# Kernel tuning notes

Hardware: AMD Instinct MI355X
Metric: run time of the kernel (lower is better)

Reference implementation:

```python
import jax, jax.numpy as jnp
import numpy as np

B, S, H = 2, 4096, 2048
NH, NKV, D = 16, 4, 128
BS, LOCAL, GLOB, STRIDE = 64, 8, 4, 16
SEL = GLOB + LOCAL
SCALE = D ** -0.5
NEG = -1e9


def rotate_half(x):
    x1, x2 = x[..., : D // 2], x[..., D // 2 :]
    return jnp.concatenate([-x2, x1], axis=-1)


def setup_inputs():
    key = jax.random.key(0)
    ks = jax.random.split(key, 5)
    hidden_states = jax.random.normal(ks[0], (B, S, H), dtype=jnp.float32)
    # standard RoPE tables, shape [B, S, D] as the module expects (cos.unsqueeze(1))
    pos = jnp.arange(S, dtype=jnp.float32)
    inv = 1.0 / (10000.0 ** (jnp.arange(0, D, 2, dtype=jnp.float32) / D))
    freqs = pos[:, None] * inv[None, :]
    emb = jnp.concatenate([freqs, freqs], axis=-1)
    cos = jnp.broadcast_to(jnp.cos(emb)[None], (B, S, D)).astype(jnp.float32)
    sin = jnp.broadcast_to(jnp.sin(emb)[None], (B, S, D)).astype(jnp.float32)
    std = 0.02
    Wq = jax.random.normal(ks[1], (NH * D, H), dtype=jnp.float32) * std
    Wk = jax.random.normal(ks[2], (NKV * D, H), dtype=jnp.float32) * std
    Wv = jax.random.normal(ks[3], (NKV * D, H), dtype=jnp.float32) * std
    Wo = jax.random.normal(ks[4], (H, NH * D), dtype=jnp.float32) * std
    return {"hidden_states": hidden_states, "cos": cos, "sin": sin,
            "Wq": Wq, "Wk": Wk, "Wv": Wv, "Wo": Wo}


def _block_sparse_attn(q, k, v):
    # q, k, v: [B, NH, S, D]; past_len = 0, attention_mask = None (all keys valid)
    qb = S // BS
    kb = S // BS
    qid = jnp.arange(qb)
    # local blocks: the LOCAL most recent blocks ending at the query block
    loc = qid[:, None] - (LOCAL - 1 - jnp.arange(LOCAL)[None, :])
    loc = jnp.clip(loc, 0, kb - 1)
    # global blocks: strided anchors
    g = jnp.clip(jnp.arange(GLOB) * STRIDE, 0, kb - 1)
    glob = jnp.broadcast_to(g[None, :], (qb, GLOB))
    sel = jnp.concatenate([glob, loc], axis=1)  # [qb, SEL]
    valid = sel <= qid[:, None]                 # causal at block level
    # dedup: drop a selected block if an earlier slot selected the same block
    eq = sel[:, :, None] == sel[:, None, :]
    lower = jnp.tril(jnp.ones((SEL, SEL), dtype=bool), k=-1)
    keep = (~(eq & lower[None]).any(-1)) & valid  # [qb, SEL]

    k_blk = k.reshape(B, NH, kb, BS, D)
    v_blk = v.reshape(B, NH, kb, BS, D)
    k_sel = jnp.take(k_blk, sel.reshape(-1), axis=2).reshape(B, NH, qb, SEL * BS, D)
    v_sel = jnp.take(v_blk, sel.reshape(-1), axis=2).reshape(B, NH, qb, SEL * BS, D)
    q_blk = q.reshape(B, NH, qb, BS, D)

    scores = jnp.einsum("bhqid,bhqjd->bhqij", q_blk, k_sel) * SCALE  # [B,NH,qb,BS,SEL*BS]
    keep_tok = jnp.broadcast_to(keep[:, :, None], (qb, SEL, BS)).reshape(qb, SEL * BS)
    scores = scores + (1.0 - keep_tok.astype(scores.dtype))[None, None, :, None, :] * NEG
    # intra-block causal mask where selected block == query block
    same = (sel == qid[:, None]).astype(scores.dtype)  # [qb, SEL]
    intra = jnp.triu(jnp.full((BS, BS), NEG, dtype=scores.dtype), k=1)
    scores6 = scores.reshape(B, NH, qb, BS, SEL, BS)
    scores6 = scores6 + intra[None, None, None, :, None, :] * same[None, None, :, None, :, None]
    scores = scores6.reshape(B, NH, qb, BS, SEL * BS)
    probs = jax.nn.softmax(scores, axis=-1)
    out = jnp.einsum("bhqij,bhqjd->bhqid", probs, v_sel)
    return out.reshape(B, NH, S, D)


def reference(hidden_states, cos, sin, Wq, Wk, Wv, Wo):
    q = (hidden_states @ Wq.T).reshape(B, S, NH, D).transpose(0, 2, 1, 3)
    k = (hidden_states @ Wk.T).reshape(B, S, NKV, D).transpose(0, 2, 1, 3)
    v = (hidden_states @ Wv.T).reshape(B, S, NKV, D).transpose(0, 2, 1, 3)
    c = cos[:, None, :, :]
    s = sin[:, None, :, :]
    q = q * c + rotate_half(q) * s
    k = k * c + rotate_half(k) * s
    rep = NH // NKV
    k = jnp.repeat(k, rep, axis=1)
    v = jnp.repeat(v, rep, axis=1)
    out = _block_sparse_attn(q, k, v)
    out = out.transpose(0, 2, 1, 3).reshape(B, S, NH * D)
    return out @ Wo.T
```

## Files before the change

kernel.cpp:

```cpp
#include <hip/hip_runtime.h>

typedef __bf16 bf16_t;
typedef __bf16 bf16x8_t __attribute__((ext_vector_type(8)));
typedef __bf16 bf16x4_t __attribute__((ext_vector_type(4)));
typedef float f32x4_t __attribute__((ext_vector_type(4)));
typedef unsigned short u16;
typedef unsigned int u32;

#define B_ 2
#define S_ 4096
#define NH_ 16
#define NKV_ 4
#define D_ 128
#define NEG_ (-1000000000.0f)
#define SCALE_ 0.08838834764831845f

__device__ __forceinline__ void load16(const bf16_t* g, bf16_t* l) {
  __builtin_amdgcn_global_load_lds(
      (__attribute__((address_space(1))) void*)(g),
      (__attribute__((address_space(3))) void*)(l),
      16, 0, 0);
}

__global__ __launch_bounds__(256) void cvt_all_kernel(const float* __restrict__ hs,
                                                      const float* __restrict__ Wq,
                                                      const float* __restrict__ Wk,
                                                      const float* __restrict__ Wv,
                                                      const float* __restrict__ Wo,
                                                      bf16_t* __restrict__ Xb,
                                                      bf16_t* __restrict__ Wb,
                                                      bf16_t* __restrict__ Wob) {
  int i = blockIdx.x * 256 + threadIdx.x;
  const float* src; bf16_t* dst; int local;
  if (i < 4194304)      { src = hs; dst = Xb;            local = i; }
  else if (i < 5242880) { src = Wq; dst = Wb;            local = i - 4194304; }
  else if (i < 5505024) { src = Wk; dst = Wb + 4194304;  local = i - 5242880; }
  else if (i < 5767168) { src = Wv; dst = Wb + 5242880;  local = i - 5505024; }
  else                  { src = Wo; dst = Wob;           local = i - 5767168; }
  float4 v = ((const float4*)src)[local];
  bf16x4_t o;
  o.x = (bf16_t)v.x; o.y = (bf16_t)v.y; o.z = (bf16_t)v.z; o.w = (bf16_t)v.w;
  *(bf16x4_t*)(dst + (size_t)local * 4) = o;
}

template <int BF16OUT>
__global__ __launch_bounds__(256) void gemm_bt_kernel(const bf16_t* __restrict__ A,
                                                      const bf16_t* __restrict__ Bm,
                                                      float* __restrict__ Cf,
                                                      bf16_t* __restrict__ Cb,
                                                      int M, int N, int K) {
  __shared__ bf16_t As[128 * 32];
  __shared__ bf16_t Bs[128 * 32];
  const int t = threadIdx.x;
  const int lane = t & 63;
  const int w = t >> 6;
  const int wr = w >> 1, wc = w & 1;
  const int l15 = lane & 15, l4 = lane >> 4;
  const int m0 = blockIdx.x * 128;
  const int n0 = blockIdx.y * 128;
  const int xr = (l15 >> 1) & 3;

  f32x4_t acc[4][4] = {};

  for (int k0 = 0; k0 < K; k0 += 32) {
    __syncthreads();
#pragma unroll
    for (int i = 0; i < 2; i++) {
      int f = t + 256 * i;
      int row = f >> 2, cl = f & 3;
      int cg = cl ^ ((row >> 1) & 3);
      load16(A + (size_t)(m0 + row) * K + k0 + cg * 8, As + (w * 64 + i * 256) * 8);
      load16(Bm + (size_t)(n0 + row) * K + k0 + cg * 8, Bs + (w * 64 + i * 256) * 8);
    }
    __syncthreads();
    bf16x8_t af[4], bfr[4];
#pragma unroll
    for (int mi = 0; mi < 4; mi++) {
      int ra = wr * 64 + mi * 16 + l15;
      af[mi] = *(const bf16x8_t*)&As[(ra * 4 + (l4 ^ xr)) * 8];
    }
#pragma unroll
    for (int ni = 0; ni < 4; ni++) {
      int rb = wc * 64 + ni * 16 + l15;
      bfr[ni] = *(const bf16x8_t*)&Bs[(rb * 4 + (l4 ^ xr)) * 8];
    }
#pragma unroll
    for (int mi = 0; mi < 4; mi++)
#pragma unroll
      for (int ni = 0; ni < 4; ni++)
        acc[mi][ni] = __builtin_amdgcn_mfma_f32_16x16x32_bf16(af[mi], bfr[ni], acc[mi][ni], 0, 0, 0);
  }

#pragma unroll
  for (int mi = 0; mi < 4; mi++)
#pragma unroll
    for (int ni = 0; ni < 4; ni++)
#pragma unroll
      for (int r = 0; r < 4; r++) {
        int grow = m0 + wr * 64 + mi * 16 + l4 * 4 + r;
        int gcol = n0 + wc * 64 + ni * 16 + l15;
        float v = acc[mi][ni][r];
        if (BF16OUT) Cb[(size_t)grow * N + gcol] = (bf16_t)v;
        else Cf[(size_t)grow * N + gcol] = v;
      }
}

__global__ __launch_bounds__(320) void rope_kernel(const bf16_t* __restrict__ qkv,
                                                   const float* __restrict__ cosp,
                                                   const float* __restrict__ sinp,
                                                   bf16_t* __restrict__ Qro,
                                                   bf16_t* __restrict__ Kro) {
  const int tk = blockIdx.x;
  const int b = tk >> 12;
  const int s = tk & 4095;
  const int sblock = s >> 6, row = s & 63;
  const int idx = threadIdx.x;
  int head, lc;
  const bf16_t* base;
  bf16_t* outp;
  if (idx < 256) {
    head = idx >> 4; lc = idx & 15;
    base = qkv + (size_t)tk * 3072 + head * 128;
    outp = Qro + ((size_t)(b * NH_ + head) * 64 + sblock) * 8192;
  } else {
    int i2 = idx - 256;
    head = i2 >> 4; lc = i2 & 15;
    base = qkv + (size_t)tk * 3072 + 2048 + head * 128;
    outp = Kro + ((size_t)(b * NKV_ + head) * 64 + sblock) * 8192;
  }
  const int d0 = lc * 8;
  bf16x8_t x = *(const bf16x8_t*)(base + d0);
  const int d0p = (d0 < 64) ? d0 + 64 : d0 - 64;
  bf16x8_t xp = *(const bf16x8_t*)(base + d0p);
  const float sgn = (d0 < 64) ? -1.0f : 1.0f;
  const float* cb = cosp + (size_t)tk * 128 + d0;
  const float* sb = sinp + (size_t)tk * 128 + d0;
  bf16x8_t o;
#pragma unroll
  for (int e = 0; e < 8; e++)
    o[e] = (bf16_t)((float)x[e] * cb[e] + sgn * (float)xp[e] * sb[e]);
  *(bf16x8_t*)(outp + (lc * 64 + row) * 8) = o;
}

__global__ __launch_bounds__(256) void vtrans_kernel(const u16* __restrict__ qkv,
                                                     u16* __restrict__ vt) {
  __shared__ u16 tile[64][136];
  const int sblock = blockIdx.x;
  const int kh = blockIdx.y;
  const int b = blockIdx.z;
  const int t = threadIdx.x;
#pragma unroll
  for (int i = 0; i < 4; i++) {
    int f = t + 256 * i;
    int sl = f >> 4, c = f & 15;
    uint4 vv = *(const uint4*)(qkv + (size_t)(b * S_ + sblock * 64 + sl) * 3072 + 2560 + kh * 128 + c * 8);
    *(uint4*)&tile[sl][c * 8] = vv;
  }
  __syncthreads();
  u16* out = vt + ((size_t)(b * NKV_ + kh) * 64 + sblock) * 8192;
#pragma unroll
  for (int i = 0; i < 4; i++) {
    int g = t + 256 * i;
    int sc = g >> 7, d = g & 127;
    u16 e0 = tile[sc * 8 + 0][d], e1 = tile[sc * 8 + 1][d];
    u16 e2 = tile[sc * 8 + 2][d], e3 = tile[sc * 8 + 3][d];
    u16 e4 = tile[sc * 8 + 4][d], e5 = tile[sc * 8 + 5][d];
    u16 e6 = tile[sc * 8 + 6][d], e7 = tile[sc * 8 + 7][d];
    uint4 ov;
    ov.x = (u32)e0 | ((u32)e1 << 16);
    ov.y = (u32)e2 | ((u32)e3 << 16);
    ov.z = (u32)e4 | ((u32)e5 << 16);
    ov.w = (u32)e6 | ((u32)e7 << 16);
    *(uint4*)(out + (size_t)g * 8) = ov;
  }
}

__global__ __launch_bounds__(256) void attn_kernel(const bf16_t* __restrict__ Qr,
                                                   const bf16_t* __restrict__ Kr,
                                                   const bf16_t* __restrict__ Vt,
                                                   bf16_t* __restrict__ Ao) {
  __shared__ bf16_t Ks[2][8192];
  __shared__ bf16_t Vs[2][8192];
  __shared__ bf16_t Ps[4 * 16 * 72];
  const int qid = blockIdx.x;
  const int kh = blockIdx.y >> 1;
  const int hp = blockIdx.y & 1;
  const int b = blockIdx.z;
  const int t = threadIdx.x;
  const int lane = t & 63;
  const int w = t >> 6;
  const int l15 = lane & 15, l4 = lane >> 4;
  const int h = kh * 4 + hp * 2 + (w >> 1);
  int row0[2];
  row0[0] = ((w * 2) & 3) * 16;
  row0[1] = ((w * 2 + 1) & 3) * 16;

  int list[12];
  int nkeep = 0;
#pragma unroll
  for (int j = 0; j < 12; j++) {
    int cj;
    if (j < 4) cj = j * 16;
    else { cj = qid - 11 + j; cj = cj < 0 ? 0 : cj; cj = cj > 63 ? 63 : cj; }
    bool keep = (cj <= qid);
#pragma unroll
    for (int i = 0; i < j; i++) {
      int ci;
      if (i < 4) ci = i * 16;
      else { ci = qid - 11 + i; ci = ci < 0 ? 0 : ci; ci = ci > 63 ? 63 : ci; }
      if (ci == cj) keep = false;
    }
    if (keep) list[nkeep++] = cj;
  }

  const bf16_t* Qg = Qr + ((size_t)(b * NH_ + h) * 64 + qid) * 8192;
  const bf16_t* Kg = Kr + ((size_t)(b * NKV_ + kh) * 64) * 8192;
  const bf16_t* Vg = Vt + ((size_t)(b * NKV_ + kh) * 64) * 8192;

  bf16x8_t qa[2][4];
#pragma unroll
  for (int mt = 0; mt < 2; mt++)
#pragma unroll
    for (int ks = 0; ks < 4; ks++)
      qa[mt][ks] = *(const bf16x8_t*)(Qg + ((ks * 4 + l4) * 64 + row0[mt] + l15) * 8);

  bf16x8_t ones;
#pragma unroll
  for (int e = 0; e < 8; e++) ones[e] = (bf16_t)1.0f;

  float mi_r[2][4], li_r[2][4];
  f32x4_t oacc[2][8] = {};
#pragma unroll
  for (int mt = 0; mt < 2; mt++)
#pragma unroll
    for (int r = 0; r < 4; r++) { mi_r[mt][r] = -__builtin_inff(); li_r[mt][r] = 0.0f; }

  {
    int cj = list[0];
#pragma unroll
    for (int i = 0; i < 4; i++) {
      int f = t + 256 * i;
      load16(Kg + (size_t)cj * 8192 + (size_t)f * 8, Ks[0] + (w * 64 + i * 256) * 8);
      load16(Vg + (size_t)cj * 8192 + (size_t)f * 8, Vs[0] + (w * 64 + i * 256) * 8);
    }
  }

  int cur = 0;
#pragma unroll 1
  for (int idx = 0; idx < nkeep; idx++) {
    const int cj = list[idx];
    __syncthreads();
    if (idx + 1 < nkeep) {
      int cn = list[idx + 1];
#pragma unroll
      for (int i = 0; i < 4; i++) {
        int f = t + 256 * i;
        load16(Kg + (size_t)cn * 8192 + (size_t)f * 8, Ks[cur ^ 1] + (w * 64 + i * 256) * 8);
        load16(Vg + (size_t)cn * 8192 + (size_t)f * 8, Vs[cur ^ 1] + (w * 64 + i * 256) * 8);
      }
    }
    const bf16_t* ks_ = Ks[cur];
    const bf16_t* vs_ = Vs[cur];

    f32x4_t sacc[2][4] = {};
#pragma unroll
    for (int ks = 0; ks < 4; ks++)
#pragma unroll
      for (int ni = 0; ni < 4; ni++) {
        bf16x8_t kb = *(const bf16x8_t*)&ks_[((ks * 4 + l4) * 64 + ni * 16 + l15) * 8];
#pragma unroll
        for (int mt = 0; mt < 2; mt++)
          sacc[mt][ni] = __builtin_amdgcn_mfma_f32_16x16x32_bf16(qa[mt][ks], kb, sacc[mt][ni], 0, 0, 0);
      }

    const bool diag = (cj == qid);
    float alpha[2][4];
#pragma unroll
    for (int mt = 0; mt < 2; mt++) {
      float sv[4][4];
#pragma unroll
      for (int ni = 0; ni < 4; ni++)
#pragma unroll
        for (int r = 0; r < 4; r++) {
          float x = sacc[mt][ni][r] * SCALE_;
          if (diag && (ni * 16 + l15) > (row0[mt] + l4 * 4 + r)) x += NEG_;
          sv[ni][r] = x;
        }

      float rmax[4];
#pragma unroll
      for (int r = 0; r < 4; r++)
        rmax[r] = fmaxf(fmaxf(sv[0][r], sv[1][r]), fmaxf(sv[2][r], sv[3][r]));
#pragma unroll
      for (int msk = 1; msk < 16; msk <<= 1)
#pragma unroll
        for (int r = 0; r < 4; r++)
          rmax[r] = fmaxf(rmax[r], __shfl_xor(rmax[r], msk, 64));
#pragma unroll
      for (int r = 0; r < 4; r++) {
        float nm = fmaxf(mi_r[mt][r], rmax[r]);
        alpha[mt][r] = __expf(mi_r[mt][r] - nm);
        mi_r[mt][r] = nm;
      }
      float p[4][4];
#pragma unroll
      for (int ni = 0; ni < 4; ni++)
#pragma unroll
        for (int r = 0; r < 4; r++)
          p[ni][r] = __expf(sv[ni][r] - mi_r[mt][r]);
#pragma unroll
      for (int ni = 0; ni < 4; ni++)
#pragma unroll
        for (int r = 0; r < 4; r++)
          Ps[w * 1152 + (l4 * 4 + r) * 72 + ni * 16 + l15] = (bf16_t)p[ni][r];
#pragma unroll
      for (int n2 = 0; n2 < 8; n2++)
#pragma unroll
        for (int r = 0; r < 4; r++)
          oacc[mt][n2][r] *= alpha[mt][r];

      f32x4_t lacc = {};
#pragma unroll
      for (int kst = 0; kst < 2; kst++) {
        bf16x8_t pa = *(const bf16x8_t*)&Ps[w * 1152 + l15 * 72 + kst * 32 + l4 * 8];
        lacc = __builtin_amdgcn_mfma_f32_16x16x32_bf16(pa, ones, lacc, 0, 0, 0);
#pragma unroll
        for (int n2 = 0; n2 < 8; n2++) {
          bf16x8_t vb = *(const bf16x8_t*)&vs_[((kst * 4 + l4) * 128 + n2 * 16 + l15) * 8];
          oacc[mt][n2] = __builtin_amdgcn_mfma_f32_16x16x32_bf16(pa, vb, oacc[mt][n2], 0, 0, 0);
        }
      }
#pragma unroll
      for (int r = 0; r < 4; r++)
        li_r[mt][r] = li_r[mt][r] * alpha[mt][r] + lacc[r];
    }

    cur ^= 1;
  }

#pragma unroll
  for (int mt = 0; mt < 2; mt++) {
    float invl[4];
#pragma unroll
    for (int r = 0; r < 4; r++) invl[r] = 1.0f / li_r[mt][r];
#pragma unroll
    for (int n2 = 0; n2 < 8; n2++)
#pragma unroll
      for (int r = 0; r < 4; r++) {
        int m = row0[mt] + l4 * 4 + r;
        size_t idx = ((size_t)(b * S_ + qid * 64 + m)) * (NH_ * D_) + h * D_ + n2 * 16 + l15;
        Ao[idx] = (bf16_t)(oacc[mt][n2][r] * invl[r]);
      }
  }
}

extern "C" void kernel_launch(void* const* d_in, const int* in_sizes, int n_in,
                              void* d_out, int out_size, void* d_ws, size_t ws_size,
                              hipStream_t stream) {
  const float* hs = (const float*)d_in[0];
  const float* cosp = (const float*)d_in[1];
  const float* sinp = (const float*)d_in[2];
  const float* Wq = (const float*)d_in[3];
  const float* Wk = (const float*)d_in[4];
  const float* Wv = (const float*)d_in[5];
  const float* Wo = (const float*)d_in[6];
  float* outp = (float*)d_out;

  char* ws = (char*)d_ws;
  bf16_t* Xb   = (bf16_t*)(ws);
  bf16_t* Wb   = (bf16_t*)(ws + 33554432);
  bf16_t* Wob  = (bf16_t*)(ws + 46137344);
  bf16_t* QKVo = (bf16_t*)(ws + 54525952);
  bf16_t* Qr   = (bf16_t*)(ws + 104857600);
  bf16_t* Kr   = (bf16_t*)(ws + 138412032);
  bf16_t* Vt   = (bf16_t*)(ws + 146800640);
  bf16_t* Ao   = QKVo;

  cvt_all_kernel<<<dim3(26624), dim3(256), 0, stream>>>(hs, Wq, Wk, Wv, Wo, Xb, Wb, Wob);

  gemm_bt_kernel<1><<<dim3(64, 24), dim3(256), 0, stream>>>(Xb, Wb, (float*)nullptr, QKVo,
                                                            8192, 3072, 2048);
  rope_kernel<<<dim3(8192), dim3(320), 0, stream>>>(QKVo, cosp, sinp, Qr, Kr);
  vtrans_kernel<<<dim3(64, NKV_, B_), dim3(256), 0, stream>>>((const u16*)QKVo, (u16*)Vt);
  attn_kernel<<<dim3(64, NKV_ * 2, B_), dim3(256), 0, stream>>>(Qr, Kr, Vt, Ao);
  gemm_bt_kernel<0><<<dim3(64, 16), dim3(256), 0, stream>>>(Ao, Wob, outp, (bf16_t*)nullptr,
                                                            8192, 2048, 2048);
}
```

Before: 531.8 us.

## Replace 128x128 GEMM with 256x256 double-buffered pipelined 8-wave kernel

Replaces the simple single-buffered 128x128 GEMM used for the QKV projection and the output projection with a 256x256-tile, 512-thread kernel. It double-buffers LDS over 64-wide K steps and interleaves global-to-LDS staging with MFMA quadrants under explicit barriers and setprio. It also remaps workgroups across XCDs so neighbouring tiles share an L2. The goal is more data reuse per tile and hiding load latency behind matrix math. In exchange it uses more registers and LDS, drops the old LDS swizzle, and relies on hand-tuned waitcnt counts that are fragile.

```diff
diff --git a/kernel.cpp b/kernel.cpp
--- a/kernel.cpp
+++ b/kernel.cpp
@@ -43,63 +43,124 @@
   *(bf16x4_t*)(dst + (size_t)local * 4) = o;
 }
 
+
+#define SB0() __builtin_amdgcn_sched_barrier(0)
+#define BAR_MID() { SB0(); __builtin_amdgcn_s_barrier(); \
+  asm volatile("s_waitcnt lgkmcnt(0)" ::: "memory"); SB0(); }
+#define BAR_END() { SB0(); __builtin_amdgcn_s_barrier(); SB0(); }
+#define BAR_END_VM() { SB0(); asm volatile("s_waitcnt vmcnt(4)" ::: "memory"); \
+  __builtin_amdgcn_s_barrier(); SB0(); }
+
+#define LDA_(BUF, MP) { \
+  _Pragma("unroll") for (int mi = 0; mi < 4; mi++) { \
+    _Pragma("unroll") for (int ks = 0; ks < 2; ks++) { \
+      a[mi][ks] = *(const bf16x8_t*)&As[BUF][ks][wr * 128 + (MP) * 64 + mi * 16 + l15][l4 * 8]; } } }
+
+#define LDB_(BUF, NP) { \
+  _Pragma("unroll") for (int n2 = 0; n2 < 2; n2++) { \
+    _Pragma("unroll") for (int ks = 0; ks < 2; ks++) { \
+      b[(NP) * 2 + n2][ks] = *(const bf16x8_t*)&Bs[BUF][ks][wc * 64 + (NP) * 32 + n2 * 16 + l15][l4 * 8]; } } }
+
+#define MFMA_Q(MP, NP) { \
+  __builtin_amdgcn_s_setprio(1); \
+  _Pragma("unroll") for (int mi = 0; mi < 4; mi++) { \
+    _Pragma("unroll") for (int n2 = 0; n2 < 2; n2++) { \
+      _Pragma("unroll") for (int ks = 0; ks < 2; ks++) { \
+        acc[(MP) * 4 + mi][(NP) * 2 + n2] = __builtin_amdgcn_mfma_f32_16x16x32_bf16( \
+            a[mi][ks], b[(NP) * 2 + n2][ks], acc[(MP) * 4 + mi][(NP) * 2 + n2], 0, 0, 0); } } } \
+  __builtin_amdgcn_s_setprio(0); }
+
 template <int BF16OUT>
-__global__ __launch_bounds__(256) void gemm_bt_kernel(const bf16_t* __restrict__ A,
-                                                      const bf16_t* __restrict__ Bm,
-                                                      float* __restrict__ Cf,
-                                                      bf16_t* __restrict__ Cb,
-                                                      int M, int N, int K) {
-  __shared__ bf16_t As[128 * 32];
-  __shared__ bf16_t Bs[128 * 32];
+__global__ __launch_bounds__(512, 2) void gemm256_kernel(const bf16_t* __restrict__ A,
+                                                         const bf16_t* __restrict__ Bm,
+                                                         float* __restrict__ Cf,
+                                                         bf16_t* __restrict__ Cb,
+                                                         int M, int N, int K) {
+  __shared__ __align__(16) bf16_t As[2][2][256][32];
+  __shared__ __align__(16) bf16_t Bs[2][2][256][32];
   const int t = threadIdx.x;
   const int lane = t & 63;
   const int w = t >> 6;
-  const int wr = w >> 1, wc = w & 1;
+  const int wr = w >> 2;
+  const int wc = w & 3;
   const int l15 = lane & 15, l4 = lane >> 4;
-  const int m0 = blockIdx.x * 128;
-  const int n0 = blockIdx.y * 128;
-  const int xr = (l15 >> 1) & 3;
-
-  f32x4_t acc[4][4] = {};
-
-  for (int k0 = 0; k0 < K; k0 += 32) {
-    __syncthreads();
-#pragma unroll
-    for (int i = 0; i < 2; i++) {
-      int f = t + 256 * i;
-      int row = f >> 2, cl = f & 3;
-      int cg = cl ^ ((row >> 1) & 3);
-      load16(A + (size_t)(m0 + row) * K + k0 + cg * 8, As + (w * 64 + i * 256) * 8);
-      load16(Bm + (size_t)(n0 + row) * K + k0 + cg * 8, Bs + (w * 64 + i * 256) * 8);
-    }
-    __syncthreads();
-    bf16x8_t af[4], bfr[4];
-#pragma unroll
-    for (int mi = 0; mi < 4; mi++) {
-      int ra = wr * 64 + mi * 16 + l15;
-      af[mi] = *(const bf16x8_t*)&As[(ra * 4 + (l4 ^ xr)) * 8];
-    }
-#pragma unroll
-    for (int ni = 0; ni < 4; ni++) {
-      int rb = wc * 64 + ni * 16 + l15;
-      bfr[ni] = *(const bf16x8_t*)&Bs[(rb * 4 + (l4 ^ xr)) * 8];
-    }
-#pragma unroll
-    for (int mi = 0; mi < 4; mi++)
-#pragma unroll
-      for (int ni = 0; ni < 4; ni++)
-        acc[mi][ni] = __builtin_amdgcn_mfma_f32_16x16x32_bf16(af[mi], bfr[ni], acc[mi][ni], 0, 0, 0);
-  }
-
-#pragma unroll
-  for (int mi = 0; mi < 4; mi++)
+  const int sp = w >> 2;
+  const int swi = w & 3;
+  const int srow = lane >> 2;
+  const int sg = lane & 3;
+
+  const int nwg = gridDim.x;
+  const int qq = nwg >> 3, rr = nwg & 7;
+  const int xcd = blockIdx.x & 7, bix = blockIdx.x >> 3;
+  const int wg = (xcd < rr ? xcd * (qq + 1) : rr * (qq + 1) + (xcd - rr) * qq) + bix;
+  const int mtiles = M >> 8;
+  const int m0 = (wg % mtiles) * 256;
+  const int n0 = (wg / mtiles) * 256;
+
+  const bf16_t* Ablk = A + (size_t)m0 * K;
+  const bf16_t* Bblk = Bm + (size_t)n0 * K;
+
+  f32x4_t acc[8][4] = {};
+  bf16x8_t a[4][2], b[4][2];
+
+  const int nkt = K >> 6;
+  const int nit = nkt >> 1;
+
+  auto stageA = [&](int buf, int mp, int kt) {
+#pragma unroll
+    for (int c = 0; c < 2; c++) {
+      int r0 = c * 128 + mp * 64;
+      load16(Ablk + (size_t)(r0 + swi * 16 + srow) * K + kt * 64 + sp * 32 + sg * 8,
+             &As[buf][0][0][0] + sp * 8192 + (r0 + swi * 16) * 32);
+    }
+  };
+  auto stageB = [&](int buf, int np, int kt) {
+#pragma unroll
+    for (int c = 0; c < 2; c++) {
+      int r0 = (c * 2 + (swi >> 1)) * 64 + np * 32 + (swi & 1) * 16;
+      load16(Bblk + (size_t)(r0 + srow) * K + kt * 64 + sp * 32 + sg * 8,
+             &Bs[buf][0][0][0] + sp * 8192 + r0 * 32);
+    }
+  };
+
+  stageA(0, 0, 0); stageB(0, 0, 0); stageA(0, 1, 0); stageB(0, 1, 0);
+  stageA(1, 0, 1); stageB(1, 0, 1);
+  asm volatile("s_waitcnt vmcnt(4)" ::: "memory");
+  __builtin_amdgcn_s_barrier();
+  SB0();
+
+#pragma unroll 1
+  for (int i = 0; i < nit; i++) {
+    const int ktA = 2 * i + 1;
+    const int ktB = (2 * i + 2 < nkt) ? 2 * i + 2 : nkt - 1;
+    const int ktC = (2 * i + 3 < nkt) ? 2 * i + 3 : nkt - 1;
+    LDA_(0, 0); LDB_(0, 0); stageA(1, 1, ktA);
+    BAR_MID(); MFMA_Q(0, 0); BAR_END();
+    LDB_(0, 1); stageB(1, 1, ktA);
+    BAR_MID(); MFMA_Q(0, 1); BAR_END();
+    LDA_(0, 1); stageA(0, 0, ktB);
+    BAR_MID(); MFMA_Q(1, 0); BAR_END();
+    stageB(0, 0, ktB);
+    BAR_MID(); MFMA_Q(1, 1); BAR_END_VM();
+    LDA_(1, 0); LDB_(1, 0); stageA(0, 1, ktB);
+    BAR_MID(); MFMA_Q(0, 0); BAR_END();
+    LDB_(1, 1); stageB(0, 1, ktB);
+    BAR_MID(); MFMA_Q(0, 1); BAR_END();
+    LDA_(1, 1); stageA(1, 0, ktC);
+    BAR_MID(); MFMA_Q(1, 0); BAR_END();
+    stageB(1, 0, ktC);
+    BAR_MID(); MFMA_Q(1, 1); BAR_END_VM();
+  }
+
+#pragma unroll
+  for (int ar = 0; ar < 8; ar++)
 #pragma unroll
     for (int ni = 0; ni < 4; ni++)
 #pragma unroll
       for (int r = 0; r < 4; r++) {
-        int grow = m0 + wr * 64 + mi * 16 + l4 * 4 + r;
+        int grow = m0 + wr * 128 + (ar >> 2) * 64 + (ar & 3) * 16 + l4 * 4 + r;
         int gcol = n0 + wc * 64 + ni * 16 + l15;
-        float v = acc[mi][ni][r];
+        float v = acc[ar][ni][r];
         if (BF16OUT) Cb[(size_t)grow * N + gcol] = (bf16_t)v;
         else Cf[(size_t)grow * N + gcol] = v;
       }
@@ -378,11 +439,11 @@
 
   cvt_all_kernel<<<dim3(26624), dim3(256), 0, stream>>>(hs, Wq, Wk, Wv, Wo, Xb, Wb, Wob);
 
-  gemm_bt_kernel<1><<<dim3(64, 24), dim3(256), 0, stream>>>(Xb, Wb, (float*)nullptr, QKVo,
-                                                            8192, 3072, 2048);
+  gemm256_kernel<1><<<dim3(384), dim3(512), 0, stream>>>(Xb, Wb, (float*)nullptr, QKVo,
+                                                         8192, 3072, 2048);
   rope_kernel<<<dim3(8192), dim3(320), 0, stream>>>(QKVo, cosp, sinp, Qr, Kr);
   vtrans_kernel<<<dim3(64, NKV_, B_), dim3(256), 0, stream>>>((const u16*)QKVo, (u16*)Vt);
   attn_kernel<<<dim3(64, NKV_ * 2, B_), dim3(256), 0, stream>>>(Qr, Kr, Vt, Ao);
-  gemm_bt_kernel<0><<<dim3(64, 16), dim3(256), 0, stream>>>(Ao, Wob, outp, (bf16_t*)nullptr,
-                                                            8192, 2048, 2048);
-}
+  gemm256_kernel<0><<<dim3(256), dim3(512), 0, stream>>>(Ao, Wob, outp, (bf16_t*)nullptr,
+                                                         8192, 2048, 2048);
+}
```

New measurement: 551.7 us. +3.7%, slower.
